# Kernel optimization log

Hardware: AMD Instinct MI355X
Metric: run time of the kernel (lower is better)

## Reference

```python
import jax, jax.numpy as jnp
import numpy as np

N = 100000      # nodes
E = 1600000     # edges (before self-loops)
IN = 64         # in_channels
HID = 16        # hidden_channels
HEADS = 4       # num_heads
G = 512         # number of graphs in batch
SLOPE = 0.2     # GATConv leaky_relu negative_slope


def setup_inputs() -> dict:
    key = jax.random.key(0)
    ks = jax.random.split(key, 12)
    s = 0.1
    x = jax.random.normal(ks[0], (N, IN), jnp.float32)
    edge_index = jax.random.randint(ks[1], (2, E), 0, N, dtype=jnp.int64)
    batch = jnp.sort(jax.random.randint(ks[2], (N,), 0, G, dtype=jnp.int64))
    W1 = jax.random.normal(ks[3], (IN, HEADS * HID), jnp.float32) * s
    a1_src = jax.random.normal(ks[4], (HEADS, HID), jnp.float32) * s
    a1_dst = jax.random.normal(ks[5], (HEADS, HID), jnp.float32) * s
    b1 = jnp.zeros((HEADS * HID,), jnp.float32)
    W2 = jax.random.normal(ks[6], (HEADS * HID, HID), jnp.float32) * s
    a2_src = jax.random.normal(ks[7], (1, HID), jnp.float32) * s
    a2_dst = jax.random.normal(ks[8], (1, HID), jnp.float32) * s
    b2 = jnp.zeros((HID,), jnp.float32)
    Wc = jax.random.normal(ks[9], (HID, 1), jnp.float32) * s
    bc = jnp.zeros((1,), jnp.float32)
    return dict(x=x, edge_index=edge_index, batch=batch, W1=W1, a1_src=a1_src,
                a1_dst=a1_dst, b1=b1, W2=W2, a2_src=a2_src, a2_dst=a2_dst,
                b2=b2, Wc=Wc, bc=bc)


def gat_layer(x, src, dst, W, a_s, a_d, bias, heads, out_ch, concat):
    # PyG GATConv: linear -> per-edge attention logits -> segment softmax over dst -> scatter aggregate
    n = x.shape[0]
    h = (x @ W).reshape(n, heads, out_ch)              # [N, H, C]
    al_s = jnp.sum(h * a_s, axis=-1)                   # [N, H]
    al_d = jnp.sum(h * a_d, axis=-1)                   # [N, H]
    e = al_s[src] + al_d[dst]                          # [E, H]
    e = jnp.where(e > 0, e, SLOPE * e)                 # leaky_relu
    m = jax.ops.segment_max(e, dst, num_segments=n)    # per-dst max (self-loops ensure non-empty)
    p = jnp.exp(e - m[dst])
    denom = jax.ops.segment_sum(p, dst, num_segments=n)
    alpha = p / (denom[dst] + 1e-16)                   # [E, H]
    out = jax.ops.segment_sum(h[src] * alpha[:, :, None], dst, num_segments=n)  # [N, H, C]
    out = out.reshape(n, heads * out_ch) if concat else out.mean(axis=1)
    return out + bias


def reference(x, edge_index, batch, W1, a1_src, a1_dst, b1, W2, a2_src, a2_dst, b2, Wc, bc):
    loops = jnp.arange(N, dtype=edge_index.dtype)      # GATConv add_self_loops=True
    src = jnp.concatenate([edge_index[0], loops])
    dst = jnp.concatenate([edge_index[1], loops])
    h = jax.nn.elu(gat_layer(x, src, dst, W1, a1_src, a1_dst, b1, HEADS, HID, True))
    # dropout inactive (eval mode)
    h = jax.nn.elu(gat_layer(h, src, dst, W2, a2_src, a2_dst, b2, 1, HID, False))
    counts = jax.ops.segment_sum(jnp.ones((N,), h.dtype), batch, num_segments=G)
    pooled = jax.ops.segment_sum(h, batch, num_segments=G) / jnp.maximum(counts, 1.0)[:, None]
    return pooled @ Wc + bc
```

## Files before the change

kernel.cpp:

```cpp
#include <hip/hip_runtime.h>
#include <hip/hip_fp16.h>
#include <hip/hip_fp8.h>

#define N_NODES 100000
#define N_EDGES 1600000
#define ET      (N_EDGES + N_NODES)
#define NG      512
#define SLOPE   0.2f

#define BKT_SHIFT 9
#define NB_B   ((N_NODES + 511) / 512)
#define CHUNK_A 8192
#define NBLK_A ((ET + CHUNK_A - 1) / CHUNK_A)
#define H1B    ((N_NODES + 255) / 256)

typedef _Float16 half8_t __attribute__((ext_vector_type(8)));
typedef float    f32x4_t __attribute__((ext_vector_type(4)));

__global__ __launch_bounds__(256) void k_prep(
    const float* __restrict__ x, const float* __restrict__ W1,
    const float* __restrict__ a1s, const float* __restrict__ a1d,
    const int* __restrict__ ei,
    __hip_fp8_e4m3* __restrict__ h1, float* __restrict__ al1s, float* __restrict__ al1d,
    int* __restrict__ bsize)
{
    __shared__ float Wl[64 * 64];
    __shared__ float asf[64], adf[64];
    __shared__ int hcnt[NB_B];
    int tid = threadIdx.x;

    if (blockIdx.x >= H1B) {
        for (int i = tid; i < NB_B; i += 256) hcnt[i] = 0;
        __syncthreads();
        int base = (blockIdx.x - H1B) * CHUNK_A;
        int m = min(CHUNK_A, ET - base);
        for (int i = tid; i < m; i += 256) {
            int eid = base + i;
            int d = (eid < N_EDGES) ? ei[N_EDGES + eid] : (eid - N_EDGES);
            atomicAdd(&hcnt[d >> BKT_SHIFT], 1);
        }
        __syncthreads();
        for (int i = tid; i < NB_B; i += 256)
            if (hcnt[i]) atomicAdd(&bsize[i], hcnt[i]);
        return;
    }

    for (int i = tid; i < 64 * 64; i += 256) Wl[i] = W1[i];
    if (tid < 64) { asf[tid] = a1s[tid]; adf[tid] = a1d[tid]; }
    __syncthreads();

    int wv = tid >> 6, lane = tid & 63;
    int m = lane & 15, q = lane >> 4;

    half8_t bf[4][2];
#pragma unroll
    for (int t = 0; t < 4; ++t)
#pragma unroll
        for (int s = 0; s < 2; ++s) {
            half8_t b;
#pragma unroll
            for (int j = 0; j < 8; ++j)
                b[j] = (_Float16)Wl[(s * 32 + q * 8 + j) * 64 + t * 16 + m];
            bf[t][s] = b;
        }

    for (int it = 0; it < 4; ++it) {
        int node0 = blockIdx.x * 256 + wv * 64 + it * 16;
        int node = node0 + m;
        half8_t av0 = {}, av1 = {};
        if (node < N_NODES) {
            const float4* xr = (const float4*)(x + (long long)node * 64);
            float4 p0 = xr[q * 2], p1 = xr[q * 2 + 1];
            float4 p2 = xr[q * 2 + 8], p3 = xr[q * 2 + 9];
            av0[0] = (_Float16)p0.x; av0[1] = (_Float16)p0.y;
            av0[2] = (_Float16)p0.z; av0[3] = (_Float16)p0.w;
            av0[4] = (_Float16)p1.x; av0[5] = (_Float16)p1.y;
            av0[6] = (_Float16)p1.z; av0[7] = (_Float16)p1.w;
            av1[0] = (_Float16)p2.x; av1[1] = (_Float16)p2.y;
            av1[2] = (_Float16)p2.z; av1[3] = (_Float16)p2.w;
            av1[4] = (_Float16)p3.x; av1[5] = (_Float16)p3.y;
            av1[6] = (_Float16)p3.z; av1[7] = (_Float16)p3.w;
        }
        f32x4_t acc[4] = {{0,0,0,0},{0,0,0,0},{0,0,0,0},{0,0,0,0}};
#pragma unroll
        for (int t = 0; t < 4; ++t) {
            acc[t] = __builtin_amdgcn_mfma_f32_16x16x32_f16(av0, bf[t][0], acc[t], 0, 0, 0);
            acc[t] = __builtin_amdgcn_mfma_f32_16x16x32_f16(av1, bf[t][1], acc[t], 0, 0, 0);
        }
#pragma unroll
        for (int r = 0; r < 4; ++r) {
            int nr = node0 + q * 4 + r;
            bool ok = nr < N_NODES;
#pragma unroll
            for (int t = 0; t < 4; ++t) {
                float v = acc[t][r];
                if (ok) h1[(long long)nr * 64 + t * 16 + m] = __hip_fp8_e4m3(v);
                float ps = v * asf[t * 16 + m];
                float pd = v * adf[t * 16 + m];
                ps += __shfl_xor(ps, 1); ps += __shfl_xor(ps, 2);
                ps += __shfl_xor(ps, 4); ps += __shfl_xor(ps, 8);
                pd += __shfl_xor(pd, 1); pd += __shfl_xor(pd, 2);
                pd += __shfl_xor(pd, 4); pd += __shfl_xor(pd, 8);
                if (ok && m == t) { al1s[nr * 4 + t] = ps; al1d[nr * 4 + t] = pd; }
            }
        }
    }
}

__global__ __launch_bounds__(256) void k_scanB(const int* __restrict__ bsize,
                                               int* __restrict__ bbase, int* __restrict__ bcur)
{
    __shared__ int tmp[256];
    int tid = threadIdx.x;
    int v = (tid < NB_B) ? bsize[tid] : 0;
    tmp[tid] = v;
    __syncthreads();
    for (int off = 1; off < 256; off <<= 1) {
        int t = (tid >= off) ? tmp[tid - off] : 0;
        __syncthreads();
        tmp[tid] += t;
        __syncthreads();
    }
    if (tid < NB_B) { int e = tmp[tid] - v; bbase[tid] = e; bcur[tid] = e; }
}

__global__ __launch_bounds__(1024) void k_passA(const int* __restrict__ ei,
                                                int* __restrict__ bcur, unsigned int* __restrict__ ebuf)
{
    __shared__ unsigned int stage[CHUNK_A];
    __shared__ unsigned char sbin[CHUNK_A];
    __shared__ int hist[NB_B];
    __shared__ int binst[NB_B];
    __shared__ int resv[NB_B];
    __shared__ int cur[NB_B];
    __shared__ int tmp[1024];
    int tid = threadIdx.x;
    int base = blockIdx.x * CHUNK_A;
    int m = min(CHUNK_A, ET - base);
    for (int i = tid; i < NB_B; i += 1024) hist[i] = 0;
    __syncthreads();
    for (int i = tid; i < m; i += 1024) {
        int eid = base + i;
        int d = (eid < N_EDGES) ? ei[N_EDGES + eid] : (eid - N_EDGES);
        atomicAdd(&hist[d >> BKT_SHIFT], 1);
    }
    __syncthreads();
    int v = (tid < NB_B) ? hist[tid] : 0;
    tmp[tid] = v;
    __syncthreads();
    for (int off = 1; off < 1024; off <<= 1) {
        int t = (tid >= off) ? tmp[tid - off] : 0;
        __syncthreads();
        tmp[tid] += t;
        __syncthreads();
    }
    if (tid < NB_B) {
        int e = tmp[tid] - v;
        binst[tid] = e;
        cur[tid] = e;
        resv[tid] = v ? atomicAdd(&bcur[tid], v) : 0;
    }
    __syncthreads();
    for (int i = tid; i < m; i += 1024) {
        int eid = base + i;
        int s, d;
        if (eid < N_EDGES) { s = ei[eid]; d = ei[N_EDGES + eid]; }
        else               { s = eid - N_EDGES; d = s; }
        int b = d >> BKT_SHIFT;
        int pos = atomicAdd(&cur[b], 1);
        stage[pos] = ((unsigned int)(d & 511) << 17) | (unsigned int)s;
        sbin[pos] = (unsigned char)b;
    }
    __syncthreads();
    for (int i = tid; i < m; i += 1024) {
        int b = sbin[i];
        ebuf[resv[b] + (i - binst[b])] = stage[i];
    }
}

__global__ __launch_bounds__(1024) void k_passB(
    const unsigned int* __restrict__ ebuf, const int* __restrict__ bbase,
    const int* __restrict__ bsize,
    int* __restrict__ csr, int* __restrict__ offs, int* __restrict__ deg)
{
    __shared__ int ldeg[512];
    __shared__ int lofs[512];
    __shared__ int lcur[512];
    int tid = threadIdx.x;
    int b = blockIdx.x;
    int nb0 = b << BKT_SHIFT;
    int nn = min(512, N_NODES - nb0);
    int gbase = bbase[b], cnt = bsize[b];
    if (tid < 512) ldeg[tid] = 0;
    __syncthreads();
    for (int i = tid; i < cnt; i += 1024)
        atomicAdd(&ldeg[ebuf[gbase + i] >> 17], 1);
    __syncthreads();
    int v = 0;
    if (tid < 512) { v = ldeg[tid]; lofs[tid] = v; }
    __syncthreads();
    for (int off = 1; off < 512; off <<= 1) {
        int t = (tid >= off && tid < 512) ? lofs[tid - off] : 0;
        __syncthreads();
        if (tid < 512) lofs[tid] += t;
        __syncthreads();
    }
    if (tid < 512) {
        int e = lofs[tid] - v;
        lcur[tid] = e;
        if (tid < nn) { offs[nb0 + tid] = gbase + e; deg[nb0 + tid] = v; }
    }
    __syncthreads();
    for (int i = tid; i < cnt; i += 1024) {
        unsigned int ev = ebuf[gbase + i];
        int dl = ev >> 17, s = (int)(ev & 0x1FFFF);
        int p = atomicAdd(&lcur[dl], 1);
        csr[gbase + p] = s;
    }
}

__global__ __launch_bounds__(256) void k_agg1(
    const int* __restrict__ offs, const int* __restrict__ deg, const int* __restrict__ csr,
    const __hip_fp8_e4m3* __restrict__ h1, const float* __restrict__ al1s, const float* __restrict__ al1d,
    const float* __restrict__ b1, __half* __restrict__ h1bg)
{
    __shared__ int   sarr[4][64];
    __shared__ float warr[4][4 * 72];
    __shared__ __align__(16) float h1b[4][64];
    int tid = threadIdx.x;
    int wv = tid >> 6, lane = tid & 63;
    int eslot = lane >> 4;
    int cq = lane & 15;
    int h = cq >> 2;
    int cq4 = cq * 4;
    int node = blockIdx.x * 4 + wv;
    int st = offs[node], dg = deg[node];
    const float4 ald4 = *(const float4*)(al1d + node * 4);
    float b1l = b1[lane];
    const char* __restrict__ h1c = (const char*)h1;

    float a0 = 0.f, a1 = 0.f, a2 = 0.f, a3 = 0.f, den = 0.f;
    for (int base = 0; base < dg; base += 64) {
        int m = min(64, dg - base);
        int s = 0;
        float w0 = 0.f, w1 = 0.f, w2 = 0.f, w3 = 0.f;
        if (lane < m) {
            s = csr[st + base + lane];
            const float4 as4 = *(const float4*)(al1s + s * 4);
            float e0 = as4.x + ald4.x; e0 = e0 > 0.f ? e0 : SLOPE * e0;
            float e1 = as4.y + ald4.y; e1 = e1 > 0.f ? e1 : SLOPE * e1;
            float e2 = as4.z + ald4.z; e2 = e2 > 0.f ? e2 : SLOPE * e2;
            float e3 = as4.w + ald4.w; e3 = e3 > 0.f ? e3 : SLOPE * e3;
            w0 = __expf(e0); w1 = __expf(e1); w2 = __expf(e2); w3 = __expf(e3);
        }
        sarr[wv][lane] = s << 6;
        warr[wv][0 * 72 + lane] = w0;
        warr[wv][1 * 72 + lane] = w1;
        warr[wv][2 * 72 + lane] = w2;
        warr[wv][3 * 72 + lane] = w3;
        int m4 = (m + 3) & ~3;
#pragma unroll 4
        for (int j0 = 0; j0 < m4; j0 += 4) {
            int j = j0 + eslot;
            int off = sarr[wv][j] + cq4;
            float wgt = warr[wv][h * 72 + j];
            unsigned int pk = *(const unsigned int*)(h1c + off);
            a0 = fmaf(wgt, __builtin_amdgcn_cvt_f32_fp8(pk, 0), a0);
            a1 = fmaf(wgt, __builtin_amdgcn_cvt_f32_fp8(pk, 1), a1);
            a2 = fmaf(wgt, __builtin_amdgcn_cvt_f32_fp8(pk, 2), a2);
            a3 = fmaf(wgt, __builtin_amdgcn_cvt_f32_fp8(pk, 3), a3);
            den += wgt;
        }
    }
    a0 += __shfl_xor(a0, 16); a0 += __shfl_xor(a0, 32);
    a1 += __shfl_xor(a1, 16); a1 += __shfl_xor(a1, 32);
    a2 += __shfl_xor(a2, 16); a2 += __shfl_xor(a2, 32);
    a3 += __shfl_xor(a3, 16); a3 += __shfl_xor(a3, 32);
    den += __shfl_xor(den, 16); den += __shfl_xor(den, 32);
    if (lane < 16)
        *(float4*)&h1b[wv][cq4] = make_float4(a0, a1, a2, a3);
    float denc = __shfl(den, (lane >> 4) << 2);
    float v = h1b[wv][lane] / (denc + 1e-16f) + b1l;
    v = v > 0.f ? v : __expf(v) - 1.f;
    h1bg[(long long)node * 64 + lane] = __float2half_rn(v);
}

__global__ __launch_bounds__(256) void k_mid(
    const __half* __restrict__ h1bg, const float* __restrict__ W2,
    const float* __restrict__ a2s, const float* __restrict__ a2d,
    __half* __restrict__ h2, float* __restrict__ al2s, float* __restrict__ al2d)
{
    __shared__ float W2l[64 * 16];
    int tid = threadIdx.x;
    for (int i = tid; i < 64 * 16; i += 256) W2l[i] = W2[i];
    __syncthreads();
    int wv = tid >> 6, lane = tid & 63;
    int m = lane & 15, q = lane >> 4;
    half8_t bf[2];
#pragma unroll
    for (int s = 0; s < 2; ++s) {
        half8_t b;
#pragma unroll
        for (int j = 0; j < 8; ++j)
            b[j] = (_Float16)W2l[(s * 32 + q * 8 + j) * 16 + m];
        bf[s] = b;
    }
    int node0 = blockIdx.x * 64 + wv * 16;
    half8_t av0 = {}, av1 = {};
    if (node0 + m < N_NODES) {
        const __half* ar = h1bg + (long long)(node0 + m) * 64;
        av0 = *(const half8_t*)(ar + q * 8);
        av1 = *(const half8_t*)(ar + 32 + q * 8);
    }
    f32x4_t acc = {0, 0, 0, 0};
    acc = __builtin_amdgcn_mfma_f32_16x16x32_f16(av0, bf[0], acc, 0, 0, 0);
    acc = __builtin_amdgcn_mfma_f32_16x16x32_f16(av1, bf[1], acc, 0, 0, 0);
    float a2sm = a2s[m], a2dm = a2d[m];
#pragma unroll
    for (int r = 0; r < 4; ++r) {
        int nr = node0 + q * 4 + r;
        bool ok = nr < N_NODES;
        float v = acc[r];
        if (ok) h2[nr * 16 + m] = __float2half_rn(v);
        float ps = v * a2sm, pd = v * a2dm;
        ps += __shfl_xor(ps, 1); ps += __shfl_xor(ps, 2);
        ps += __shfl_xor(ps, 4); ps += __shfl_xor(ps, 8);
        pd += __shfl_xor(pd, 1); pd += __shfl_xor(pd, 2);
        pd += __shfl_xor(pd, 4); pd += __shfl_xor(pd, 8);
        if (ok && m == 0) { al2s[nr] = ps; al2d[nr] = pd; }
    }
}

__global__ __launch_bounds__(256) void k_agg2(
    const int* __restrict__ offs, const int* __restrict__ deg, const int* __restrict__ csr,
    const __half* __restrict__ h2, const float* __restrict__ al2s, const float* __restrict__ al2d,
    const float* __restrict__ b2, float* __restrict__ hout)
{
    __shared__ int   sarr[4][64];
    __shared__ float warr[4][64];
    int tid = threadIdx.x;
    int wv = tid >> 6, lane = tid & 63;
    int ec = lane >> 3, cc = lane & 7;
    int node = blockIdx.x * 4 + wv;
    int st = offs[node], dg = deg[node];
    float ald = al2d[node];
    const __half2* __restrict__ h2v = (const __half2*)h2;

    float a0 = 0.f, a1 = 0.f, den = 0.f;
    for (int base = 0; base < dg; base += 64) {
        int m = min(64, dg - base);
        int s = 0; float wl = 0.f;
        if (lane < m) {
            s = csr[st + base + lane];
            float e = al2s[s] + ald;
            e = e > 0.f ? e : SLOPE * e;
            wl = __expf(e);
        }
        sarr[wv][lane] = s;
        warr[wv][lane] = wl;
        float t = wl;
#pragma unroll
        for (int x = 1; x < 64; x <<= 1) t += __shfl_xor(t, x);
        den += t;
        int m8 = (m + 7) & ~7;
#pragma unroll 2
        for (int j0 = 0; j0 < m8; j0 += 8) {
            int j = j0 + ec;
            int s2i = sarr[wv][j];
            float wgt = warr[wv][j];
            __half2 hv = h2v[s2i * 8 + cc];
            a0 = fmaf(__low2float(hv), wgt, a0);
            a1 = fmaf(__high2float(hv), wgt, a1);
        }
    }
    a0 += __shfl_xor(a0, 8);  a1 += __shfl_xor(a1, 8);
    a0 += __shfl_xor(a0, 16); a1 += __shfl_xor(a1, 16);
    a0 += __shfl_xor(a0, 32); a1 += __shfl_xor(a1, 32);
    if (lane < 8) {
        float inv = 1.f / (den + 1e-16f);
        float v0 = a0 * inv + b2[2 * cc];
        float v1 = a1 * inv + b2[2 * cc + 1];
        v0 = v0 > 0.f ? v0 : __expf(v0) - 1.f;
        v1 = v1 > 0.f ? v1 : __expf(v1) - 1.f;
        ((float2*)hout)[node * 8 + cc] = make_float2(v0, v1);
    }
}

__global__ __launch_bounds__(256) void k_pool(
    const float* __restrict__ hout, const int* __restrict__ batch,
    const float* __restrict__ Wc, const float* __restrict__ bc, float* __restrict__ out)
{
    __shared__ float red[16][17];
    __shared__ int bnd[2];
    int g = blockIdx.x;
    int t = threadIdx.x, c = t & 15, slot = t >> 4;
    if (t < 2) {
        int key = g + t;
        int lo = 0, hi = N_NODES;
        while (lo < hi) { int mid = (lo + hi) >> 1; if (batch[mid] < key) lo = mid + 1; else hi = mid; }
        bnd[t] = lo;
    }
    __syncthreads();
    int s = bnd[0], e = bnd[1];
    float sum = 0.f;
    for (int n = s + slot; n < e; n += 16)
        sum += hout[n * 16 + c];
    red[slot][c] = sum;
    __syncthreads();
    if (t < 16) {
        float tot = 0.f;
#pragma unroll
        for (int k = 0; k < 16; ++k) tot += red[k][t];
        float cnt = fmaxf((float)(e - s), 1.0f);
        float pc = (tot / cnt) * Wc[t];
        pc += __shfl_xor(pc, 1); pc += __shfl_xor(pc, 2);
        pc += __shfl_xor(pc, 4); pc += __shfl_xor(pc, 8);
        if (t == 0) out[g] = pc + bc[0];
    }
}

extern "C" void kernel_launch(void* const* d_in, const int* in_sizes, int n_in,
                              void* d_out, int out_size, void* d_ws, size_t ws_size,
                              hipStream_t stream)
{
    const float* x    = (const float*)d_in[0];
    const int*   ei   = (const int*)d_in[1];
    const int*   batc = (const int*)d_in[2];
    const float* W1   = (const float*)d_in[3];
    const float* a1s  = (const float*)d_in[4];
    const float* a1d  = (const float*)d_in[5];
    const float* b1   = (const float*)d_in[6];
    const float* W2   = (const float*)d_in[7];
    const float* a2s  = (const float*)d_in[8];
    const float* a2d  = (const float*)d_in[9];
    const float* b2   = (const float*)d_in[10];
    const float* Wc   = (const float*)d_in[11];
    const float* bc   = (const float*)d_in[12];
    float* out = (float*)d_out;

    char* ws = (char*)d_ws;
    size_t off = 0;
    auto carveB = [&](size_t bytes) {
        void* p = ws + off;
        off += ((bytes + 15) & ~(size_t)15);
        return p;
    };
    auto carve = [&](size_t elems) { return carveB(elems * 4); };
    int*   bsize  = (int*)  carve(NB_B);
    size_t zero_bytes = off;
    int*   bbase  = (int*)  carve(NB_B);
    int*   bcur   = (int*)  carve(NB_B);
    unsigned int* ebuf = (unsigned int*)carve(ET);
    int*   csr    = (int*)  carve(ET);
    int*   offs   = (int*)  carve(N_NODES);
    int*   deg    = (int*)  carve(N_NODES);
    __hip_fp8_e4m3* h1 = (__hip_fp8_e4m3*)carveB((size_t)N_NODES * 64);
    float* al1s   = (float*)carve((size_t)N_NODES * 4);
    float* al1d   = (float*)carve((size_t)N_NODES * 4);
    __half* h1bg  = (__half*)carveB((size_t)N_NODES * 64 * 2);
    __half* h2    = (__half*)carveB((size_t)N_NODES * 16 * 2);
    float* al2s   = (float*)carve(N_NODES);
    float* al2d   = (float*)carve(N_NODES);
    float* hout   = (float*)carve((size_t)N_NODES * 16);

    hipMemsetAsync(d_ws, 0, zero_bytes, stream);

    k_prep <<<H1B + NBLK_A, 256, 0, stream>>>(x, W1, a1s, a1d, ei, h1, al1s, al1d, bsize);
    k_scanB<<<1, 256, 0, stream>>>(bsize, bbase, bcur);
    k_passA<<<NBLK_A, 1024, 0, stream>>>(ei, bcur, ebuf);
    k_passB<<<NB_B, 1024, 0, stream>>>(ebuf, bbase, bsize, csr, offs, deg);
    k_agg1 <<<N_NODES / 4, 256, 0, stream>>>(offs, deg, csr, h1, al1s, al1d, b1, h1bg);
    k_mid  <<<(N_NODES + 63) / 64, 256, 0, stream>>>(h1bg, W2, a2s, a2d, h2, al2s, al2d);
    k_agg2 <<<N_NODES / 4, 256, 0, stream>>>(offs, deg, csr, h2, al2s, al2d,
                                             b2, hout);
    k_pool <<<NG, 256, 0, stream>>>(hout, batc, Wc, bc, out);
}
```

Measured before the change: 260.8 us.

## Process four destination nodes per wavefront in both GAT aggregation kernels

Each wavefront in k_agg1 and k_agg2 now handles four consecutive destination nodes and walks their concatenated CSR edge range in 64-edge chunks, instead of one node per wavefront. Each edge is mapped to its node by comparing against prefix degree offsets, with per-node accumulators kept separately. This targets the lanes left idle when a node's degree (about 17 on average) is well below 64, and it cuts the grid size by four. In exchange it adds per-node masking and loop overhead, and uses more registers for the four sets of accumulators. It relies on the CSR segments of consecutive nodes being contiguous.

Measured after the change: 258.1 us. No clear change (-1.0%).

```diff
diff --git a/kernel.cpp b/kernel.cpp
--- a/kernel.cpp
+++ b/kernel.cpp
@@ -226,63 +226,85 @@
 {
     __shared__ int   sarr[4][64];
     __shared__ float warr[4][4 * 72];
-    __shared__ __align__(16) float h1b[4][64];
+    __shared__ __align__(16) float h1b[4][4][64];
     int tid = threadIdx.x;
     int wv = tid >> 6, lane = tid & 63;
     int eslot = lane >> 4;
     int cq = lane & 15;
     int h = cq >> 2;
     int cq4 = cq * 4;
-    int node = blockIdx.x * 4 + wv;
-    int st = offs[node], dg = deg[node];
-    const float4 ald4 = *(const float4*)(al1d + node * 4);
-    float b1l = b1[lane];
+    int node0 = (blockIdx.x * 4 + wv) * 4;
+    int dg0 = deg[node0], dg1 = deg[node0 + 1], dg2 = deg[node0 + 2], dg3 = deg[node0 + 3];
+    int st0 = offs[node0];
+    int e1 = dg0, e2 = e1 + dg1, e3 = e2 + dg2, D = e3 + dg3;
+    float bias = b1[lane];
     const char* __restrict__ h1c = (const char*)h1;
 
-    float a0 = 0.f, a1 = 0.f, a2 = 0.f, a3 = 0.f, den = 0.f;
-    for (int base = 0; base < dg; base += 64) {
-        int m = min(64, dg - base);
+    float A0[4] = {0,0,0,0}, A1[4] = {0,0,0,0}, A2[4] = {0,0,0,0}, A3[4] = {0,0,0,0};
+    float DN[4] = {0,0,0,0};
+    for (int base = 0; base < D; base += 64) {
+        int m = min(64, D - base);
         int s = 0;
         float w0 = 0.f, w1 = 0.f, w2 = 0.f, w3 = 0.f;
         if (lane < m) {
-            s = csr[st + base + lane];
+            int e = base + lane;
+            s = csr[st0 + e];
+            int nid = (e >= e1) + (e >= e2) + (e >= e3);
             const float4 as4 = *(const float4*)(al1s + s * 4);
-            float e0 = as4.x + ald4.x; e0 = e0 > 0.f ? e0 : SLOPE * e0;
-            float e1 = as4.y + ald4.y; e1 = e1 > 0.f ? e1 : SLOPE * e1;
-            float e2 = as4.z + ald4.z; e2 = e2 > 0.f ? e2 : SLOPE * e2;
-            float e3 = as4.w + ald4.w; e3 = e3 > 0.f ? e3 : SLOPE * e3;
-            w0 = __expf(e0); w1 = __expf(e1); w2 = __expf(e2); w3 = __expf(e3);
+            const float4 ad4 = *(const float4*)(al1d + (node0 + nid) * 4);
+            float q0 = as4.x + ad4.x; q0 = q0 > 0.f ? q0 : SLOPE * q0;
+            float q1 = as4.y + ad4.y; q1 = q1 > 0.f ? q1 : SLOPE * q1;
+            float q2 = as4.z + ad4.z; q2 = q2 > 0.f ? q2 : SLOPE * q2;
+            float q3 = as4.w + ad4.w; q3 = q3 > 0.f ? q3 : SLOPE * q3;
+            w0 = __expf(q0); w1 = __expf(q1); w2 = __expf(q2); w3 = __expf(q3);
         }
         sarr[wv][lane] = s << 6;
         warr[wv][0 * 72 + lane] = w0;
         warr[wv][1 * 72 + lane] = w1;
         warr[wv][2 * 72 + lane] = w2;
         warr[wv][3 * 72 + lane] = w3;
-        int m4 = (m + 3) & ~3;
-#pragma unroll 4
-        for (int j0 = 0; j0 < m4; j0 += 4) {
-            int j = j0 + eslot;
-            int off = sarr[wv][j] + cq4;
-            float wgt = warr[wv][h * 72 + j];
-            unsigned int pk = *(const unsigned int*)(h1c + off);
-            a0 = fmaf(wgt, __builtin_amdgcn_cvt_f32_fp8(pk, 0), a0);
-            a1 = fmaf(wgt, __builtin_amdgcn_cvt_f32_fp8(pk, 1), a1);
-            a2 = fmaf(wgt, __builtin_amdgcn_cvt_f32_fp8(pk, 2), a2);
-            a3 = fmaf(wgt, __builtin_amdgcn_cvt_f32_fp8(pk, 3), a3);
-            den += wgt;
-        }
-    }
-    a0 += __shfl_xor(a0, 16); a0 += __shfl_xor(a0, 32);
-    a1 += __shfl_xor(a1, 16); a1 += __shfl_xor(a1, 32);
-    a2 += __shfl_xor(a2, 16); a2 += __shfl_xor(a2, 32);
-    a3 += __shfl_xor(a3, 16); a3 += __shfl_xor(a3, 32);
-    den += __shfl_xor(den, 16); den += __shfl_xor(den, 32);
-    if (lane < 16)
-        *(float4*)&h1b[wv][cq4] = make_float4(a0, a1, a2, a3);
-    float denc = __shfl(den, (lane >> 4) << 2);
-    float v = h1b[wv][lane] / (denc + 1e-16f) + b1l;
-    v = v > 0.f ? v : __expf(v) - 1.f;
-    h1bg[(long long)node * 64 + lane] = __float2half_rn(v);
+        int lo = base, hi = base + m;
+#pragma unroll
+        for (int nid = 0; nid < 4; ++nid) {
+            int jb = (nid == 0) ? 0  : ((nid == 1) ? e1 : ((nid == 2) ? e2 : e3));
+            int je = (nid == 0) ? e1 : ((nid == 1) ? e2 : ((nid == 2) ? e3 : D));
+            int js = jb > lo ? jb : lo;
+            int jeX = je < hi ? je : hi;
+            if (js < jeX) {
+                int jend = jeX - base;
+                for (int j0 = (js - base) & ~3; j0 < jend; j0 += 4) {
+                    int j = j0 + eslot;
+                    int jc = j < 63 ? j : 63;
+                    int jg = base + j;
+                    bool okv = (jg >= js) && (jg < jeX);
+                    float wgt = warr[wv][h * 72 + jc];
+                    wgt = okv ? wgt : 0.f;
+                    int off = sarr[wv][jc] + cq4;
+                    unsigned int pk = *(const unsigned int*)(h1c + off);
+                    A0[nid] = fmaf(wgt, __builtin_amdgcn_cvt_f32_fp8(pk, 0), A0[nid]);
+                    A1[nid] = fmaf(wgt, __builtin_amdgcn_cvt_f32_fp8(pk, 1), A1[nid]);
+                    A2[nid] = fmaf(wgt, __builtin_amdgcn_cvt_f32_fp8(pk, 2), A2[nid]);
+                    A3[nid] = fmaf(wgt, __builtin_amdgcn_cvt_f32_fp8(pk, 3), A3[nid]);
+                    DN[nid] += wgt;
+                }
+            }
+        }
+    }
+#pragma unroll
+    for (int nid = 0; nid < 4; ++nid) {
+        float x0 = A0[nid], x1 = A1[nid], x2 = A2[nid], x3 = A3[nid], dn = DN[nid];
+        x0 += __shfl_xor(x0, 16); x0 += __shfl_xor(x0, 32);
+        x1 += __shfl_xor(x1, 16); x1 += __shfl_xor(x1, 32);
+        x2 += __shfl_xor(x2, 16); x2 += __shfl_xor(x2, 32);
+        x3 += __shfl_xor(x3, 16); x3 += __shfl_xor(x3, 32);
+        dn += __shfl_xor(dn, 16); dn += __shfl_xor(dn, 32);
+        if (lane < 16)
+            *(float4*)&h1b[wv][nid][cq4] = make_float4(x0, x1, x2, x3);
+        float denc = __shfl(dn, (lane >> 4) << 2);
+        float v = h1b[wv][nid][lane] / (denc + 1e-16f) + bias;
+        v = v > 0.f ? v : __expf(v) - 1.f;
+        h1bg[(long long)(node0 + nid) * 64 + lane] = __float2half_rn(v);
+    }
 }
 
 __global__ __launch_bounds__(256) void k_mid(
@@ -341,48 +363,65 @@
     int tid = threadIdx.x;
     int wv = tid >> 6, lane = tid & 63;
     int ec = lane >> 3, cc = lane & 7;
-    int node = blockIdx.x * 4 + wv;
-    int st = offs[node], dg = deg[node];
-    float ald = al2d[node];
+    int node0 = (blockIdx.x * 4 + wv) * 4;
+    int dg0 = deg[node0], dg1 = deg[node0 + 1], dg2 = deg[node0 + 2], dg3 = deg[node0 + 3];
+    int st0 = offs[node0];
+    int e1 = dg0, e2 = e1 + dg1, e3 = e2 + dg2, D = e3 + dg3;
     const __half2* __restrict__ h2v = (const __half2*)h2;
 
-    float a0 = 0.f, a1 = 0.f, den = 0.f;
-    for (int base = 0; base < dg; base += 64) {
-        int m = min(64, dg - base);
+    float A0[4] = {0,0,0,0}, A1[4] = {0,0,0,0}, DN[4] = {0,0,0,0};
+    for (int base = 0; base < D; base += 64) {
+        int m = min(64, D - base);
         int s = 0; float wl = 0.f;
         if (lane < m) {
-            s = csr[st + base + lane];
-            float e = al2s[s] + ald;
-            e = e > 0.f ? e : SLOPE * e;
-            wl = __expf(e);
+            int e = base + lane;
+            s = csr[st0 + e];
+            int nid = (e >= e1) + (e >= e2) + (e >= e3);
+            float q = al2s[s] + al2d[node0 + nid];
+            q = q > 0.f ? q : SLOPE * q;
+            wl = __expf(q);
         }
         sarr[wv][lane] = s;
         warr[wv][lane] = wl;
-        float t = wl;
-#pragma unroll
-        for (int x = 1; x < 64; x <<= 1) t += __shfl_xor(t, x);
-        den += t;
-        int m8 = (m + 7) & ~7;
-#pragma unroll 2
-        for (int j0 = 0; j0 < m8; j0 += 8) {
-            int j = j0 + ec;
-            int s2i = sarr[wv][j];
-            float wgt = warr[wv][j];
-            __half2 hv = h2v[s2i * 8 + cc];
-            a0 = fmaf(__low2float(hv), wgt, a0);
-            a1 = fmaf(__high2float(hv), wgt, a1);
-        }
-    }
-    a0 += __shfl_xor(a0, 8);  a1 += __shfl_xor(a1, 8);
-    a0 += __shfl_xor(a0, 16); a1 += __shfl_xor(a1, 16);
-    a0 += __shfl_xor(a0, 32); a1 += __shfl_xor(a1, 32);
-    if (lane < 8) {
-        float inv = 1.f / (den + 1e-16f);
-        float v0 = a0 * inv + b2[2 * cc];
-        float v1 = a1 * inv + b2[2 * cc + 1];
-        v0 = v0 > 0.f ? v0 : __expf(v0) - 1.f;
-        v1 = v1 > 0.f ? v1 : __expf(v1) - 1.f;
-        ((float2*)hout)[node * 8 + cc] = make_float2(v0, v1);
+        int lo = base, hi = base + m;
+#pragma unroll
+        for (int nid = 0; nid < 4; ++nid) {
+            int jb = (nid == 0) ? 0  : ((nid == 1) ? e1 : ((nid == 2) ? e2 : e3));
+            int je = (nid == 0) ? e1 : ((nid == 1) ? e2 : ((nid == 2) ? e3 : D));
+            int js = jb > lo ? jb : lo;
+            int jeX = je < hi ? je : hi;
+            if (js < jeX) {
+                int jend = jeX - base;
+                for (int j0 = (js - base) & ~7; j0 < jend; j0 += 8) {
+                    int j = j0 + ec;
+                    int jc = j < 63 ? j : 63;
+                    int jg = base + j;
+                    bool okv = (jg >= js) && (jg < jeX);
+                    float wgt = warr[wv][jc];
+                    wgt = okv ? wgt : 0.f;
+                    int s2i = sarr[wv][jc];
+                    __half2 hv = h2v[s2i * 8 + cc];
+                    A0[nid] = fmaf(__low2float(hv),  wgt, A0[nid]);
+                    A1[nid] = fmaf(__high2float(hv), wgt, A1[nid]);
+                    DN[nid] += wgt;
+                }
+            }
+        }
+    }
+#pragma unroll
+    for (int nid = 0; nid < 4; ++nid) {
+        float x0 = A0[nid], x1 = A1[nid], dn = DN[nid];
+        x0 += __shfl_xor(x0, 8);  x1 += __shfl_xor(x1, 8);  dn += __shfl_xor(dn, 8);
+        x0 += __shfl_xor(x0, 16); x1 += __shfl_xor(x1, 16); dn += __shfl_xor(dn, 16);
+        x0 += __shfl_xor(x0, 32); x1 += __shfl_xor(x1, 32); dn += __shfl_xor(dn, 32);
+        if (lane < 8) {
+            float inv = 1.f / (dn + 1e-16f);
+            float v0 = x0 * inv + b2[2 * cc];
+            float v1 = x1 * inv + b2[2 * cc + 1];
+            v0 = v0 > 0.f ? v0 : __expf(v0) - 1.f;
+            v1 = v1 > 0.f ? v1 : __expf(v1) - 1.f;
+            ((float2*)hout)[(node0 + nid) * 8 + cc] = make_float2(v0, v1);
+        }
     }
 }
 
@@ -469,9 +508,8 @@
     k_scanB<<<1, 256, 0, stream>>>(bsize, bbase, bcur);
     k_passA<<<NBLK_A, 1024, 0, stream>>>(ei, bcur, ebuf);
     k_passB<<<NB_B, 1024, 0, stream>>>(ebuf, bbase, bsize, csr, offs, deg);
-    k_agg1 <<<N_NODES / 4, 256, 0, stream>>>(offs, deg, csr, h1, al1s, al1d, b1, h1bg);
+    k_agg1 <<<N_NODES / 16, 256, 0, stream>>>(offs, deg, csr, h1, al1s, al1d, b1, h1bg);
     k_mid  <<<(N_NODES + 63) / 64, 256, 0, stream>>>(h1bg, W2, a2s, a2d, h2, al2s, al2d);
-    k_agg2 <<<N_NODES / 4, 256, 0, stream>>>(offs, deg, csr, h2, al2s, al2d,
-                                             b2, hout);
+    k_agg2 <<<N_NODES / 16, 256, 0, stream>>>(offs, deg, csr, h2, al2s, al2d, b2, hout);
     k_pool <<<NG, 256, 0, stream>>>(hout, batc, Wc, bc, out);
 }
```
